# Optimization experiments

Measured on AMD Instinct MI355X. Metric: run time of the kernel, lower is better.

The kernel has to match this reference:

```python
import jax, jax.numpy as jnp
import numpy as np

N, E, NG = 50000, 800000, 256          # nodes, edges, graphs
NODE, EDGE, HID, OUT = 64, 16, 64, 1   # feature dims
NUM_LAYERS = 3


def _lin(key, fan_in, fan_out):
    # torch Linear default init: U(-1/sqrt(fan_in), 1/sqrt(fan_in))
    kw, kb = jax.random.split(key)
    bound = 1.0 / np.sqrt(fan_in)
    W = jax.random.uniform(kw, (fan_in, fan_out), jnp.float32, -bound, bound)
    b = jax.random.uniform(kb, (fan_out,), jnp.float32, -bound, bound)
    return W, b


def setup_inputs() -> dict:
    key = jax.random.key(0)
    ks = jax.random.split(key, 8)
    x = jax.random.normal(ks[0], (N, NODE), jnp.float32)
    edge_attr = jax.random.normal(ks[1], (E, EDGE), jnp.float32)
    edge_index = jax.random.randint(ks[2], (2, E), 0, N, dtype=jnp.int32)
    batch = jnp.sort(jax.random.randint(ks[3], (N,), 0, NG, dtype=jnp.int32))
    W_nh, b_nh = _lin(ks[4], NODE, HID)                 # node_to_hidden
    W_mh, b_mh = _lin(ks[5], 2 * HID + EDGE, HID)       # message_to_hidden
    W_om, b_om = _lin(ks[6], 2 * HID + NODE, HID)       # outMsgLin
    W_out, b_out = _lin(ks[7], HID, OUT)                # outLin
    return {"x": x, "edge_attr": edge_attr,
            "W_nh": W_nh, "b_nh": b_nh, "W_mh": W_mh, "b_mh": b_mh,
            "W_om": W_om, "b_om": b_om, "W_out": W_out, "b_out": b_out,
            "edge_index": edge_index, "batch": batch}


def reference(x, edge_attr, W_nh, b_nh, W_mh, b_mh, W_om, b_om, W_out, b_out,
              edge_index, batch):
    # h0 = relu(node_to_hidden(x))
    h0 = jax.nn.relu(x @ W_nh + b_nh)                      # [N, HID]

    # add_self_loops: append N self edges, self-loop edge_attr filled with 1.0
    self_idx = jnp.arange(N, dtype=edge_index.dtype)
    src = jnp.concatenate([edge_index[0], self_idx])       # x_j index (source)
    dst = jnp.concatenate([edge_index[1], self_idx])       # x_i index (target)
    ea = jnp.concatenate([edge_attr,
                          jnp.ones((N, EDGE), edge_attr.dtype)], axis=0)

    # MPN: num_layers of gather-concat -> scatter-add -> linear + h0 -> relu
    h = h0
    for _ in range(NUM_LAYERS):
        msg = jnp.concatenate([h[dst], h[src], ea], axis=1)        # [E+N, 2H+EDGE]
        agg = jax.ops.segment_sum(msg, dst, num_segments=N)        # [N, 2H+EDGE]
        h = jax.nn.relu(agg @ W_mh + b_mh + h0)                    # [N, HID]

    # outMsg: message = concat[h_i, h_j, x_j], aggr add, update identity
    out_msg = jnp.concatenate([h[dst], h[src], x[src]], axis=1)    # [E+N, 2H+NODE]
    agg2 = jax.ops.segment_sum(out_msg, dst, num_segments=N)       # [N, 2H+NODE]

    out = jax.nn.relu(agg2 @ W_om + b_om)                          # [N, HID]
    pooled = jax.ops.segment_sum(out, batch, num_segments=NG)      # [NG, HID]
    return pooled @ W_out + b_out                                  # [NG, OUT]
```

## Files before the change

### kernel.cpp

```cpp
#include <hip/hip_runtime.h>
#include <hip/hip_fp16.h>

#define N_NODES 50000
#define N_EDGES 800000
#define NGRAPH  256
#define FDIM    64
#define EDIM    16
#define NT      (N_NODES / 16)
#define SH      8
#define M8      (N_NODES * SH)
#define NB8     ((M8 + 255) / 256)
#define CH8     ((NB8 + 255) / 256)
#define NBG     ((N_NODES + 31) / 32)

#define GRPS       8
#define GRP_BLOCKS 256
#define GRID_CF    (GRPS * GRP_BLOCKS)
#define NPG        ((N_NODES + GRPS - 1) / GRPS)

#define SRC_SHARD(s) ((s) >> 13)

using half8  = __attribute__((ext_vector_type(8))) _Float16;
using float4v = __attribute__((ext_vector_type(4))) float;

__device__ __forceinline__ unsigned hadd2u(unsigned a, unsigned b) {
    __half2 r = __hadd2(__builtin_bit_cast(__half2, a), __builtin_bit_cast(__half2, b));
    return __builtin_bit_cast(unsigned, r);
}
__device__ __forceinline__ unsigned hmul2u(unsigned a, __half2 m) {
    __half2 r = __hmul2(__builtin_bit_cast(__half2, a), m);
    return __builtin_bit_cast(unsigned, r);
}


__global__ __launch_bounds__(256) void k_count(const int* __restrict__ src,
                                               const int* __restrict__ dst,
                                               int* __restrict__ cnt8) {
    int grp = blockIdx.x & (GRPS - 1);
    int bi  = blockIdx.x >> 3;
    int lo = grp * NPG;
    int hi = lo + NPG; if (hi > N_NODES) hi = N_NODES;
    for (int e = bi * 256 + threadIdx.x; e < N_EDGES; e += GRP_BLOCKS * 256) {
        int d = dst[e];
        if (d >= lo && d < hi) atomicAdd(&cnt8[d * SH + SRC_SHARD(src[e])], 1);
    }
}

__global__ void k_cvt_x(const float* __restrict__ x, __half* __restrict__ x16) {
    int t = blockIdx.x * blockDim.x + threadIdx.x;
    if (t < N_NODES * FDIM) x16[t] = __float2half(x[t]);
}

__global__ void k_blksum(const int* __restrict__ cnt8, int* __restrict__ blksum) {
    __shared__ int red[4];
    int b = blockIdx.x, t = threadIdx.x;
    int idx = b * 256 + t;
    int s = (idx < M8) ? cnt8[idx] : 0;
#pragma unroll
    for (int off = 32; off > 0; off >>= 1) s += __shfl_down(s, off, 64);
    int lane = t & 63, wid = t >> 6;
    if (lane == 0) red[wid] = s;
    __syncthreads();
    if (t == 0) blksum[b] = red[0] + red[1] + red[2] + red[3];
}

__global__ void k_scanblk(const int* __restrict__ blksum, int* __restrict__ boff,
                          int* __restrict__ rowp8) {
    __shared__ int sh[256];
    int t = threadIdx.x;
    int base = t * CH8;
    int v[CH8];
    int s = 0;
#pragma unroll
    for (int i = 0; i < CH8; i++) {
        int idx = base + i;
        v[i] = (idx < NB8) ? blksum[idx] : 0;
        s += v[i];
    }
    sh[t] = s;
    __syncthreads();
    for (int off = 1; off < 256; off <<= 1) {
        int u = (t >= off) ? sh[t - off] : 0;
        __syncthreads();
        sh[t] += u;
        __syncthreads();
    }
    int run = (t == 0) ? 0 : sh[t - 1];
#pragma unroll
    for (int i = 0; i < CH8; i++) {
        int idx = base + i;
        if (idx < NB8) boff[idx] = run;
        run += v[i];
    }
    if (t == 255) rowp8[M8] = sh[255];
}

__global__ void k_rowp(const int* __restrict__ cnt8, const int* __restrict__ boff,
                       int* __restrict__ rowp8, int* __restrict__ cur8) {
    __shared__ int sh[256];
    int b = blockIdx.x, t = threadIdx.x;
    int idx = b * 256 + t;
    int v = (idx < M8) ? cnt8[idx] : 0;
    sh[t] = v;
    __syncthreads();
    for (int off = 1; off < 256; off <<= 1) {
        int u = (t >= off) ? sh[t - off] : 0;
        __syncthreads();
        sh[t] += u;
        __syncthreads();
    }
    if (idx < M8) {
        int excl = sh[t] - v + boff[b];
        rowp8[idx] = excl;
        cur8[idx]  = excl;
    }
}

__global__ void k_degf(const int* __restrict__ rowp8, float* __restrict__ degf) {
    int i = blockIdx.x * blockDim.x + threadIdx.x;
    if (i < N_NODES) degf[i] = (float)(rowp8[(i + 1) * SH] - rowp8[i * SH] + 1);
}

__global__ __launch_bounds__(256) void k_fill(const int* __restrict__ src,
                                              const int* __restrict__ dst,
                                              int* __restrict__ cur8,
                                              int* __restrict__ colsrc,
                                              int* __restrict__ coledge) {
    int grp = blockIdx.x & (GRPS - 1);
    int bi  = blockIdx.x >> 3;
    int lo = grp * NPG;
    int hi = lo + NPG; if (hi > N_NODES) hi = N_NODES;
    for (int e = bi * 256 + threadIdx.x; e < N_EDGES; e += GRP_BLOCKS * 256) {
        int d = dst[e];
        if (d >= lo && d < hi) {
            int s = src[e];
            int pos = atomicAdd(&cur8[d * SH + SRC_SHARD(s)], 1);
            colsrc[pos]  = s;
            coledge[pos] = e;
        }
    }
}


__global__ __launch_bounds__(256, 8) void k_gather(
    const __half* __restrict__ h16,
    const int* __restrict__ rowp8, const int* __restrict__ colsrc,
    __half* __restrict__ agg16) {
    int lane = threadIdx.x & 63, wid = threadIdx.x >> 6;
    int g = lane >> 3;
    int c = lane & 7;
    const uint4* h8 = (const uint4*)h16;
    int node = (blockIdx.x * 4 + wid) * 8 + g;
    if (node >= N_NODES) return;
    int beg = rowp8[node * SH], end = rowp8[(node + 1) * SH];
    float a0 = 0, a1 = 0, a2 = 0, a3 = 0, a4 = 0, a5 = 0, a6 = 0, a7 = 0;
    for (int p = beg; p < end; p += 8) {
        int cidx = p + c; if (cidx > end - 1) cidx = end - 1;
        int vj = colsrc[cidx];
#pragma unroll
        for (int k = 0; k < 8; k++) {
            int j = __shfl(vj, g * 8 + k, 64);
            if (p + k < end) {
                uint4 v = h8[(size_t)j * 8 + c];
                float2 f0 = __half22float2(__builtin_bit_cast(__half2, v.x));
                float2 f1 = __half22float2(__builtin_bit_cast(__half2, v.y));
                float2 f2 = __half22float2(__builtin_bit_cast(__half2, v.z));
                float2 f3 = __half22float2(__builtin_bit_cast(__half2, v.w));
                a0 += f0.x; a1 += f0.y; a2 += f1.x; a3 += f1.y;
                a4 += f2.x; a5 += f2.y; a6 += f3.x; a7 += f3.y;
            }
        }
    }
    uint4 o;
    o.x = __builtin_bit_cast(unsigned, __floats2half2_rn(a0, a1));
    o.y = __builtin_bit_cast(unsigned, __floats2half2_rn(a2, a3));
    o.z = __builtin_bit_cast(unsigned, __floats2half2_rn(a4, a5));
    o.w = __builtin_bit_cast(unsigned, __floats2half2_rn(a6, a7));
    ((uint4*)agg16)[(size_t)node * 8 + c] = o;
}

__global__ __launch_bounds__(256, 8) void k_gxea(
    const __half* __restrict__ h16, const float* __restrict__ edge_attr,
    const int* __restrict__ rowp8, const int* __restrict__ colsrc,
    const int* __restrict__ coledge,
    __half* __restrict__ agg16, float* __restrict__ ea) {
    int lane = threadIdx.x & 63, wid = threadIdx.x >> 6;
    int g = lane >> 3;
    int c = lane & 7;
    const uint4* h8 = (const uint4*)h16;
    const float2* a2p = (const float2*)edge_attr;
    int node = (blockIdx.x * 4 + wid) * 8 + g;
    if (node >= N_NODES) return;
    int beg = rowp8[node * SH], end = rowp8[(node + 1) * SH];
    float a0 = 0, a1 = 0, a2 = 0, a3 = 0, a4 = 0, a5 = 0, a6 = 0, a7 = 0;
    float x0 = 0.f, x1 = 0.f;
    for (int p = beg; p < end; p += 8) {
        int cidx = p + c; if (cidx > end - 1) cidx = end - 1;
        int vs = colsrc[cidx];
        int ve = coledge[cidx];
#pragma unroll
        for (int k = 0; k < 8; k++) {
            int j = __shfl(vs, g * 8 + k, 64);
            int e = __shfl(ve, g * 8 + k, 64);
            if (p + k < end) {
                uint4 v = h8[(size_t)j * 8 + c];
                float2 w = a2p[(size_t)e * 8 + c];
                float2 f0 = __half22float2(__builtin_bit_cast(__half2, v.x));
                float2 f1 = __half22float2(__builtin_bit_cast(__half2, v.y));
                float2 f2 = __half22float2(__builtin_bit_cast(__half2, v.z));
                float2 f3 = __half22float2(__builtin_bit_cast(__half2, v.w));
                a0 += f0.x; a1 += f0.y; a2 += f1.x; a3 += f1.y;
                a4 += f2.x; a5 += f2.y; a6 += f3.x; a7 += f3.y;
                x0 += w.x; x1 += w.y;
            }
        }
    }
    uint4 o;
    o.x = __builtin_bit_cast(unsigned, __floats2half2_rn(a0, a1));
    o.y = __builtin_bit_cast(unsigned, __floats2half2_rn(a2, a3));
    o.z = __builtin_bit_cast(unsigned, __floats2half2_rn(a4, a5));
    o.w = __builtin_bit_cast(unsigned, __floats2half2_rn(a6, a7));
    ((uint4*)agg16)[(size_t)node * 8 + c] = o;
    ((float2*)ea)[(size_t)node * 8 + c] = make_float2(x0, x1);
}

__global__ void k_h0base(const float* __restrict__ x, const float* __restrict__ ea,
                         const float* __restrict__ Wnh, const float* __restrict__ bnh,
                         const float* __restrict__ Wmh, const float* __restrict__ bmh,
                         __half* __restrict__ h0out16, __half* __restrict__ base16) {
    __shared__ __align__(16) float sx[4][FDIM];
    __shared__ __align__(16) float sea[4][EDIM];
    int lane = threadIdx.x & 63;
    int wid  = threadIdx.x >> 6;
    float wnh[FDIM], w3[EDIM];
#pragma unroll
    for (int m = 0; m < FDIM; m++) wnh[m] = Wnh[m * FDIM + lane];
    float csum = 0.f;
#pragma unroll
    for (int m = 0; m < EDIM; m++) {
        w3[m] = Wmh[(2 * FDIM + m) * FDIM + lane];
        csum += w3[m];
    }
    float bnhk = bnh[lane], bmhk = bmh[lane];
    int gw = blockIdx.x * 4 + wid;
    int nw = gridDim.x * 4;
    for (int i = gw; i < N_NODES; i += nw) {
        sx[wid][lane] = x[i * FDIM + lane];
        if (lane < EDIM) sea[wid][lane] = ea[i * EDIM + lane];
        float acc0 = bnhk, acc1 = 0.f, acc2 = 0.f, acc3 = 0.f;
        const float4* s4 = (const float4*)sx[wid];
#pragma unroll
        for (int m4 = 0; m4 < FDIM / 4; m4++) {
            float4 v = s4[m4];
            acc0 = fmaf(v.x, wnh[4 * m4 + 0], acc0);
            acc1 = fmaf(v.y, wnh[4 * m4 + 1], acc1);
            acc2 = fmaf(v.z, wnh[4 * m4 + 2], acc2);
            acc3 = fmaf(v.w, wnh[4 * m4 + 3], acc3);
        }
        float h0 = fmaxf((acc0 + acc2) + (acc1 + acc3), 0.f);
        float b0 = h0 + bmhk + csum, b1 = 0.f, b2 = 0.f, b3 = 0.f;
        const float4* e4 = (const float4*)sea[wid];
#pragma unroll
        for (int m4 = 0; m4 < EDIM / 4; m4++) {
            float4 v = e4[m4];
            b0 = fmaf(v.x, w3[4 * m4 + 0], b0);
            b1 = fmaf(v.y, w3[4 * m4 + 1], b1);
            b2 = fmaf(v.z, w3[4 * m4 + 2], b2);
            b3 = fmaf(v.w, w3[4 * m4 + 3], b3);
        }
        h0out16[i * FDIM + lane] = __float2half(h0);
        base16[i * FDIM + lane]  = __float2half((b0 + b2) + (b1 + b3));
    }
}

#define SROW 136

__global__ __launch_bounds__(256, 4) void k_mv_mfma(
    const __half* __restrict__ agg16, const __half* __restrict__ hin16,
    const __half* __restrict__ base16, const float* __restrict__ degf,
    const float* __restrict__ Wmh, __half* __restrict__ hout16) {
    __shared__ __align__(16) _Float16 S[4][16 * SROW];
    int lane = threadIdx.x & 63, wid = threadIdx.x >> 6;
    int n = lane & 15, quad = lane >> 4;
    half8 bfr[4][4];
#pragma unroll
    for (int kk = 0; kk < 4; kk++)
#pragma unroll
        for (int nn = 0; nn < 4; nn++) {
            half8 tmp;
#pragma unroll
            for (int j = 0; j < 8; j++) {
                int kp = kk * 32 + quad * 8 + j;
                int krow = (kp < 64) ? (64 + kp) : (kp - 64);
                tmp[j] = (_Float16)Wmh[krow * FDIM + nn * 16 + n];
            }
            bfr[kk][nn] = tmp;
        }
    int t = blockIdx.x * 4 + wid;
    if (t >= NT) return;
    int tb = t * 16;
    {
        int m = lane >> 2, c = lane & 3;
        int node = tb + m;
        const uint4* ag4 = (const uint4*)agg16;
        const uint4* hh4 = (const uint4*)hin16;
        uint4 agA = ag4[(size_t)node * 8 + c * 2];
        uint4 agB = ag4[(size_t)node * 8 + c * 2 + 1];
        uint4 hA  = hh4[(size_t)node * 8 + c * 2];
        uint4 hB  = hh4[(size_t)node * 8 + c * 2 + 1];
        __half dh = __float2half(degf[node]);
        __half2 dh2 = __halves2half2(dh, dh);
        uint4 s2A, s2B, s1A, s1B;
        s2A.x = hadd2u(agA.x, hA.x); s2A.y = hadd2u(agA.y, hA.y);
        s2A.z = hadd2u(agA.z, hA.z); s2A.w = hadd2u(agA.w, hA.w);
        s2B.x = hadd2u(agB.x, hB.x); s2B.y = hadd2u(agB.y, hB.y);
        s2B.z = hadd2u(agB.z, hB.z); s2B.w = hadd2u(agB.w, hB.w);
        s1A.x = hmul2u(hA.x, dh2); s1A.y = hmul2u(hA.y, dh2);
        s1A.z = hmul2u(hA.z, dh2); s1A.w = hmul2u(hA.w, dh2);
        s1B.x = hmul2u(hB.x, dh2); s1B.y = hmul2u(hB.y, dh2);
        s1B.z = hmul2u(hB.z, dh2); s1B.w = hmul2u(hB.w, dh2);
        uint4* Sw = (uint4*)(&S[wid][m * SROW]);
        Sw[c * 2]     = s2A;
        Sw[c * 2 + 1] = s2B;
        Sw[8 + c * 2]     = s1A;
        Sw[8 + c * 2 + 1] = s1B;
    }
    float4v acc[4];
#pragma unroll
    for (int nn = 0; nn < 4; nn++)
#pragma unroll
        for (int r = 0; r < 4; r++)
            acc[nn][r] = __half2float(base16[(size_t)(tb + quad * 4 + r) * FDIM + nn * 16 + n]);
    const _Float16* Sr = S[wid];
#pragma unroll
    for (int kk = 0; kk < 4; kk++) {
        half8 a = *(const half8*)(Sr + (lane & 15) * SROW + kk * 32 + quad * 8);
#pragma unroll
        for (int nn = 0; nn < 4; nn++)
            acc[nn] = __builtin_amdgcn_mfma_f32_16x16x32_f16(a, bfr[kk][nn], acc[nn], 0, 0, 0);
    }
#pragma unroll
    for (int nn = 0; nn < 4; nn++)
#pragma unroll
        for (int r = 0; r < 4; r++)
            hout16[(size_t)(tb + quad * 4 + r) * FDIM + nn * 16 + n] =
                __float2half(fmaxf(acc[nn][r], 0.f));
}

__global__ __launch_bounds__(256, 4) void k_out_mv_mfma(
    const __half* __restrict__ agg16, const __half* __restrict__ hin16,
    const __half* __restrict__ obase16, const float* __restrict__ degf,
    const float* __restrict__ Wom, const float* __restrict__ Wout,
    float* __restrict__ sc) {
    __shared__ __align__(16) _Float16 S[4][16 * SROW];
    int lane = threadIdx.x & 63, wid = threadIdx.x >> 6;
    int n = lane & 15, quad = lane >> 4;
    half8 bfr[4][4];
#pragma unroll
    for (int kk = 0; kk < 4; kk++)
#pragma unroll
        for (int nn = 0; nn < 4; nn++) {
            half8 tmp;
#pragma unroll
            for (int j = 0; j < 8; j++) {
                int kp = kk * 32 + quad * 8 + j;
                int krow = (kp < 64) ? (64 + kp) : (kp - 64);
                tmp[j] = (_Float16)Wom[krow * FDIM + nn * 16 + n];
            }
            bfr[kk][nn] = tmp;
        }
    float wo0 = Wout[n], wo1 = Wout[16 + n], wo2 = Wout[32 + n], wo3 = Wout[48 + n];
    int t = blockIdx.x * 4 + wid;
    if (t >= NT) return;
    int tb = t * 16;
    {
        int m = lane >> 2, c = lane & 3;
        int node = tb + m;
        const uint4* ag4 = (const uint4*)agg16;
        const uint4* hh4 = (const uint4*)hin16;
        uint4 agA = ag4[(size_t)node * 8 + c * 2];
        uint4 agB = ag4[(size_t)node * 8 + c * 2 + 1];
        uint4 hA  = hh4[(size_t)node * 8 + c * 2];
        uint4 hB  = hh4[(size_t)node * 8 + c * 2 + 1];
        __half dh = __float2half(degf[node]);
        __half2 dh2 = __halves2half2(dh, dh);
        uint4 s2A, s2B, s1A, s1B;
        s2A.x = hadd2u(agA.x, hA.x); s2A.y = hadd2u(agA.y, hA.y);
        s2A.z = hadd2u(agA.z, hA.z); s2A.w = hadd2u(agA.w, hA.w);
        s2B.x = hadd2u(agB.x, hB.x); s2B.y = hadd2u(agB.y, hB.y);
        s2B.z = hadd2u(agB.z, hB.z); s2B.w = hadd2u(agB.w, hB.w);
        s1A.x = hmul2u(hA.x, dh2); s1A.y = hmul2u(hA.y, dh2);
        s1A.z = hmul2u(hA.z, dh2); s1A.w = hmul2u(hA.w, dh2);
        s1B.x = hmul2u(hB.x, dh2); s1B.y = hmul2u(hB.y, dh2);
        s1B.z = hmul2u(hB.z, dh2); s1B.w = hmul2u(hB.w, dh2);
        uint4* Sw = (uint4*)(&S[wid][m * SROW]);
        Sw[c * 2]     = s2A;
        Sw[c * 2 + 1] = s2B;
        Sw[8 + c * 2]     = s1A;
        Sw[8 + c * 2 + 1] = s1B;
    }
    float4v acc[4];
#pragma unroll
    for (int nn = 0; nn < 4; nn++)
#pragma unroll
        for (int r = 0; r < 4; r++)
            acc[nn][r] = __half2float(obase16[(size_t)(tb + quad * 4 + r) * FDIM + nn * 16 + n]);
    const _Float16* Sr = S[wid];
#pragma unroll
    for (int kk = 0; kk < 4; kk++) {
        half8 a = *(const half8*)(Sr + (lane & 15) * SROW + kk * 32 + quad * 8);
#pragma unroll
        for (int nn = 0; nn < 4; nn++)
            acc[nn] = __builtin_amdgcn_mfma_f32_16x16x32_f16(a, bfr[kk][nn], acc[nn], 0, 0, 0);
    }
#pragma unroll
    for (int r = 0; r < 4; r++) {
        float s = fmaxf(acc[0][r], 0.f) * wo0 + fmaxf(acc[1][r], 0.f) * wo1
                + fmaxf(acc[2][r], 0.f) * wo2 + fmaxf(acc[3][r], 0.f) * wo3;
        s += __shfl_xor(s, 1, 64);
        s += __shfl_xor(s, 2, 64);
        s += __shfl_xor(s, 4, 64);
        s += __shfl_xor(s, 8, 64);
        if (n == 0) sc[tb + quad * 4 + r] = s;
    }
}

#define SROW2 72
__global__ __launch_bounds__(256, 4) void k_obase_mfma(
    const __half* __restrict__ aggX16, const __half* __restrict__ x16,
    const float* __restrict__ Wom, const float* __restrict__ bom,
    __half* __restrict__ obase16) {
    __shared__ __align__(16) _Float16 S[4][16 * SROW2];
    int lane = threadIdx.x & 63, wid = threadIdx.x >> 6;
    int n = lane & 15, quad = lane >> 4;
    half8 bfr[2][4];
#pragma unroll
    for (int kk = 0; kk < 2; kk++)
#pragma unroll
        for (int nn = 0; nn < 4; nn++) {
            half8 tmp;
#pragma unroll
            for (int j = 0; j < 8; j++) {
                int kp = kk * 32 + quad * 8 + j;
                tmp[j] = (_Float16)Wom[(128 + kp) * FDIM + nn * 16 + n];
            }
            bfr[kk][nn] = tmp;
        }
    float bom_n[4];
#pragma unroll
    for (int nn = 0; nn < 4; nn++) bom_n[nn] = bom[nn * 16 + n];
    int t = blockIdx.x * 4 + wid;
    if (t >= NT) return;
    int tb = t * 16;
    {
        int m = lane >> 2, c = lane & 3;
        int node = tb + m;
        const uint4* ag4 = (const uint4*)aggX16;
        const uint4* xx4 = (const uint4*)x16;
        uint4 agA = ag4[(size_t)node * 8 + c * 2];
        uint4 agB = ag4[(size_t)node * 8 + c * 2 + 1];
        uint4 xA  = xx4[(size_t)node * 8 + c * 2];
        uint4 xB  = xx4[(size_t)node * 8 + c * 2 + 1];
        uint4 sA, sB;
        sA.x = hadd2u(agA.x, xA.x); sA.y = hadd2u(agA.y, xA.y);
        sA.z = hadd2u(agA.z, xA.z); sA.w = hadd2u(agA.w, xA.w);
        sB.x = hadd2u(agB.x, xB.x); sB.y = hadd2u(agB.y, xB.y);
        sB.z = hadd2u(agB.z, xB.z); sB.w = hadd2u(agB.w, xB.w);
        uint4* Sw = (uint4*)(&S[wid][m * SROW2]);
        Sw[c * 2]     = sA;
        Sw[c * 2 + 1] = sB;
    }
    float4v acc[4];
#pragma unroll
    for (int nn = 0; nn < 4; nn++)
#pragma unroll
        for (int r = 0; r < 4; r++) acc[nn][r] = bom_n[nn];
    const _Float16* Sr = S[wid];
#pragma unroll
    for (int kk = 0; kk < 2; kk++) {
        half8 a = *(const half8*)(Sr + (lane & 15) * SROW2 + kk * 32 + quad * 8);
#pragma unroll
        for (int nn = 0; nn < 4; nn++)
            acc[nn] = __builtin_amdgcn_mfma_f32_16x16x32_f16(a, bfr[kk][nn], acc[nn], 0, 0, 0);
    }
#pragma unroll
    for (int nn = 0; nn < 4; nn++)
#pragma unroll
        for (int r = 0; r < 4; r++)
            obase16[(size_t)(tb + quad * 4 + r) * FDIM + nn * 16 + n] =
                __float2half(acc[nn][r]);
}

__global__ void k_pool(const float* __restrict__ sc, const int* __restrict__ batch,
                       const float* __restrict__ b_out, float* __restrict__ out) {
    __shared__ float red[4];
    int g = blockIdx.x, t = threadIdx.x;
    int lo = 0, hi = N_NODES;
    while (lo < hi) { int mid = (lo + hi) >> 1; if (batch[mid] < g) lo = mid + 1; else hi = mid; }
    int lo2 = lo, hi2 = N_NODES;
    while (lo2 < hi2) { int mid = (lo2 + hi2) >> 1; if (batch[mid] < g + 1) lo2 = mid + 1; else hi2 = mid; }
    float s = 0.f;
    for (int i = lo + t; i < lo2; i += 256) s += sc[i];
#pragma unroll
    for (int off = 32; off > 0; off >>= 1) s += __shfl_down(s, off, 64);
    int lane = t & 63, wid = t >> 6;
    if (lane == 0) red[wid] = s;
    __syncthreads();
    if (t == 0) out[g] = red[0] + red[1] + red[2] + red[3] + b_out[0];
}


extern "C" void kernel_launch(void* const* d_in, const int* in_sizes, int n_in,
                              void* d_out, int out_size, void* d_ws, size_t ws_size,
                              hipStream_t stream) {
    const float* x         = (const float*)d_in[0];
    const float* edge_attr = (const float*)d_in[1];
    const float* Wnh       = (const float*)d_in[2];
    const float* bnh       = (const float*)d_in[3];
    const float* Wmh       = (const float*)d_in[4];
    const float* bmh       = (const float*)d_in[5];
    const float* Wom       = (const float*)d_in[6];
    const float* bom       = (const float*)d_in[7];
    const float* Wout      = (const float*)d_in[8];
    const float* bout      = (const float*)d_in[9];
    const int*   eidx      = (const int*)d_in[10];
    const int*   batch     = (const int*)d_in[11];
    const int*   srcI = eidx;
    const int*   dstI = eidx + N_EDGES;
    float* out = (float*)d_out;
    (void)in_sizes; (void)n_in; (void)out_size;

    char* w = (char*)d_ws;
    size_t off = 0;
    auto take = [&](size_t b) -> void* {
        void* p = w + off;
        off = (off + b + 255) & ~(size_t)255;
        return p;
    };
    float*  ea     = (float*)take((size_t)N_NODES * EDIM * 4);
    int*    cnt8   = (int*)take((size_t)M8 * 4);
    int*    rowp8  = (int*)take((size_t)(M8 + 1) * 4);
    int*    cur8   = (int*)take((size_t)M8 * 4);
    float*  degf   = (float*)take((size_t)N_NODES * 4);
    int*    colsrc = (int*)take((size_t)N_EDGES * 4);
    int*    coledge= (int*)take((size_t)N_EDGES * 4);
    float*  sc     = (float*)take((size_t)N_NODES * 4);
    int*    blks   = (int*)take((size_t)NB8 * 4);
    int*    boff   = (int*)take((size_t)NB8 * 4);
    __half* x16    = (__half*)take((size_t)N_NODES * FDIM * 2);
    __half* hA16   = (__half*)take((size_t)N_NODES * FDIM * 2);
    __half* hB16   = (__half*)take((size_t)N_NODES * FDIM * 2);
    __half* agg16  = (__half*)take((size_t)N_NODES * FDIM * 2);
    __half* base16 = (__half*)take((size_t)N_NODES * FDIM * 2);
    __half* obase16= (__half*)take((size_t)N_NODES * FDIM * 2);
    (void)ws_size;

    const int MVG = (NT + 3) / 4;
    const int GBG = (NBG + 0);

    hipMemsetAsync(cnt8, 0, (size_t)M8 * 4, stream);
    k_count<<<GRID_CF, 256, 0, stream>>>(srcI, dstI, cnt8);
    k_cvt_x<<<(N_NODES * FDIM + 255) / 256, 256, 0, stream>>>(x, x16);
    k_blksum<<<NB8, 256, 0, stream>>>(cnt8, blks);
    k_scanblk<<<1, 256, 0, stream>>>(blks, boff, rowp8);
    k_rowp<<<NB8, 256, 0, stream>>>(cnt8, boff, rowp8, cur8);
    k_degf<<<(N_NODES + 255) / 256, 256, 0, stream>>>(rowp8, degf);
    k_fill<<<GRID_CF, 256, 0, stream>>>(srcI, dstI, cur8, colsrc, coledge);

    k_gxea<<<GBG, 256, 0, stream>>>(x16, edge_attr, rowp8, colsrc, coledge,
                                    agg16, ea);
    k_obase_mfma<<<MVG, 256, 0, stream>>>(agg16, x16, Wom, bom, obase16);
    k_h0base<<<2048, 256, 0, stream>>>(x, ea, Wnh, bnh, Wmh, bmh, hA16, base16);

    k_gather<<<GBG, 256, 0, stream>>>(hA16, rowp8, colsrc, agg16);
    k_mv_mfma<<<MVG, 256, 0, stream>>>(agg16, hA16, base16, degf, Wmh, hB16);

    k_gather<<<GBG, 256, 0, stream>>>(hB16, rowp8, colsrc, agg16);
    k_mv_mfma<<<MVG, 256, 0, stream>>>(agg16, hB16, base16, degf, Wmh, hA16);

    k_gather<<<GBG, 256, 0, stream>>>(hA16, rowp8, colsrc, agg16);
    k_mv_mfma<<<MVG, 256, 0, stream>>>(agg16, hA16, base16, degf, Wmh, hB16);

    k_gather<<<GBG, 256, 0, stream>>>(hB16, rowp8, colsrc, agg16);
    k_out_mv_mfma<<<MVG, 256, 0, stream>>>(agg16, hB16, obase16, degf, Wom, Wout, sc);
    k_pool<<<NGRAPH, 256, 0, stream>>>(sc, batch, bout, out);
}
```

Baseline: 363.7 us.

## Fuse neighbor gather into MFMA linear kernels, dropping the agg buffer

Merges each gather kernel with the MFMA matvec that follows it, so a wave aggregates neighbor features for its 16-node tile straight into shared memory and then runs the matmul. This removes the round trip of the agg16 intermediate through global memory and cuts five kernel launches. In exchange, the gather phase now runs at the occupancy limit set for the MFMA kernel (launch bounds 4 instead of 8) and with fewer waves overall, which may weaken latency hiding for the irregular gathers. The aggregate is also added in fp32 before a single rounding to fp16, rather than being rounded first and then added in fp16.

```diff
diff --git a/kernel.cpp b/kernel.cpp
--- a/kernel.cpp
+++ b/kernel.cpp
@@ -11,7 +11,6 @@
 #define M8      (N_NODES * SH)
 #define NB8     ((M8 + 255) / 256)
 #define CH8     ((NB8 + 255) / 256)
-#define NBG     ((N_NODES + 31) / 32)
 
 #define GRPS       8
 #define GRP_BLOCKS 256
@@ -30,6 +29,9 @@
 __device__ __forceinline__ unsigned hmul2u(unsigned a, __half2 m) {
     __half2 r = __hmul2(__builtin_bit_cast(__half2, a), m);
     return __builtin_bit_cast(unsigned, r);
+}
+__device__ __forceinline__ unsigned packf2(float a, float b) {
+    return __builtin_bit_cast(unsigned, __floats2half2_rn(a, b));
 }
 
 
@@ -141,87 +143,298 @@
     }
 }
 
-
-__global__ __launch_bounds__(256, 8) void k_gather(
-    const __half* __restrict__ h16,
+#define SROW 136
+
+__global__ __launch_bounds__(256, 4) void k_gmv(
+    const __half* __restrict__ hin16,
     const int* __restrict__ rowp8, const int* __restrict__ colsrc,
-    __half* __restrict__ agg16) {
+    const __half* __restrict__ base16, const float* __restrict__ degf,
+    const float* __restrict__ Wmh, __half* __restrict__ hout16) {
+    __shared__ __align__(16) _Float16 S[4][16 * SROW];
     int lane = threadIdx.x & 63, wid = threadIdx.x >> 6;
+    int t = blockIdx.x * 4 + wid;
+    if (t >= NT) return;
+    int tb = t * 16;
     int g = lane >> 3;
     int c = lane & 7;
-    const uint4* h8 = (const uint4*)h16;
-    int node = (blockIdx.x * 4 + wid) * 8 + g;
-    if (node >= N_NODES) return;
-    int beg = rowp8[node * SH], end = rowp8[(node + 1) * SH];
-    float a0 = 0, a1 = 0, a2 = 0, a3 = 0, a4 = 0, a5 = 0, a6 = 0, a7 = 0;
-    for (int p = beg; p < end; p += 8) {
-        int cidx = p + c; if (cidx > end - 1) cidx = end - 1;
-        int vj = colsrc[cidx];
-#pragma unroll
-        for (int k = 0; k < 8; k++) {
-            int j = __shfl(vj, g * 8 + k, 64);
-            if (p + k < end) {
-                uint4 v = h8[(size_t)j * 8 + c];
-                float2 f0 = __half22float2(__builtin_bit_cast(__half2, v.x));
-                float2 f1 = __half22float2(__builtin_bit_cast(__half2, v.y));
-                float2 f2 = __half22float2(__builtin_bit_cast(__half2, v.z));
-                float2 f3 = __half22float2(__builtin_bit_cast(__half2, v.w));
-                a0 += f0.x; a1 += f0.y; a2 += f1.x; a3 += f1.y;
-                a4 += f2.x; a5 += f2.y; a6 += f3.x; a7 += f3.y;
+    const uint4* h8 = (const uint4*)hin16;
+
+#pragma unroll
+    for (int pass = 0; pass < 2; pass++) {
+        int m = pass * 8 + g;
+        int node = tb + m;
+        int beg = rowp8[node * SH], end = rowp8[(node + 1) * SH];
+        float a0 = 0, a1 = 0, a2 = 0, a3 = 0, a4 = 0, a5 = 0, a6 = 0, a7 = 0;
+        for (int p = beg; p < end; p += 8) {
+            int cidx = p + c; if (cidx > end - 1) cidx = end - 1;
+            int vj = colsrc[cidx];
+#pragma unroll
+            for (int k = 0; k < 8; k++) {
+                int j = __shfl(vj, g * 8 + k, 64);
+                if (p + k < end) {
+                    uint4 v = h8[(size_t)j * 8 + c];
+                    float2 f0 = __half22float2(__builtin_bit_cast(__half2, v.x));
+                    float2 f1 = __half22float2(__builtin_bit_cast(__half2, v.y));
+                    float2 f2 = __half22float2(__builtin_bit_cast(__half2, v.z));
+                    float2 f3 = __half22float2(__builtin_bit_cast(__half2, v.w));
+                    a0 += f0.x; a1 += f0.y; a2 += f1.x; a3 += f1.y;
+                    a4 += f2.x; a5 += f2.y; a6 += f3.x; a7 += f3.y;
+                }
             }
         }
-    }
-    uint4 o;
-    o.x = __builtin_bit_cast(unsigned, __floats2half2_rn(a0, a1));
-    o.y = __builtin_bit_cast(unsigned, __floats2half2_rn(a2, a3));
-    o.z = __builtin_bit_cast(unsigned, __floats2half2_rn(a4, a5));
-    o.w = __builtin_bit_cast(unsigned, __floats2half2_rn(a6, a7));
-    ((uint4*)agg16)[(size_t)node * 8 + c] = o;
-}
-
-__global__ __launch_bounds__(256, 8) void k_gxea(
-    const __half* __restrict__ h16, const float* __restrict__ edge_attr,
+        uint4 hv = h8[(size_t)node * 8 + c];
+        float dg = degf[node];
+        __half dh = __float2half(dg);
+        __half2 dh2 = __halves2half2(dh, dh);
+        float2 f0 = __half22float2(__builtin_bit_cast(__half2, hv.x));
+        float2 f1 = __half22float2(__builtin_bit_cast(__half2, hv.y));
+        float2 f2 = __half22float2(__builtin_bit_cast(__half2, hv.z));
+        float2 f3 = __half22float2(__builtin_bit_cast(__half2, hv.w));
+        uint4 s2, s1;
+        s2.x = packf2(a0 + f0.x, a1 + f0.y);
+        s2.y = packf2(a2 + f1.x, a3 + f1.y);
+        s2.z = packf2(a4 + f2.x, a5 + f2.y);
+        s2.w = packf2(a6 + f3.x, a7 + f3.y);
+        s1.x = hmul2u(hv.x, dh2); s1.y = hmul2u(hv.y, dh2);
+        s1.z = hmul2u(hv.z, dh2); s1.w = hmul2u(hv.w, dh2);
+        uint4* Sw = (uint4*)(&S[wid][m * SROW]);
+        Sw[c]     = s2;
+        Sw[8 + c] = s1;
+    }
+
+    int n = lane & 15, quad = lane >> 4;
+    half8 bfr[4][4];
+#pragma unroll
+    for (int kk = 0; kk < 4; kk++)
+#pragma unroll
+        for (int nn = 0; nn < 4; nn++) {
+            half8 tmp;
+#pragma unroll
+            for (int j = 0; j < 8; j++) {
+                int kp = kk * 32 + quad * 8 + j;
+                int krow = (kp < 64) ? (64 + kp) : (kp - 64);
+                tmp[j] = (_Float16)Wmh[krow * FDIM + nn * 16 + n];
+            }
+            bfr[kk][nn] = tmp;
+        }
+    float4v acc[4];
+#pragma unroll
+    for (int nn = 0; nn < 4; nn++)
+#pragma unroll
+        for (int r = 0; r < 4; r++)
+            acc[nn][r] = __half2float(base16[(size_t)(tb + quad * 4 + r) * FDIM + nn * 16 + n]);
+    const _Float16* Sr = S[wid];
+#pragma unroll
+    for (int kk = 0; kk < 4; kk++) {
+        half8 a = *(const half8*)(Sr + n * SROW + kk * 32 + quad * 8);
+#pragma unroll
+        for (int nn = 0; nn < 4; nn++)
+            acc[nn] = __builtin_amdgcn_mfma_f32_16x16x32_f16(a, bfr[kk][nn], acc[nn], 0, 0, 0);
+    }
+#pragma unroll
+    for (int nn = 0; nn < 4; nn++)
+#pragma unroll
+        for (int r = 0; r < 4; r++)
+            hout16[(size_t)(tb + quad * 4 + r) * FDIM + nn * 16 + n] =
+                __float2half(fmaxf(acc[nn][r], 0.f));
+}
+
+__global__ __launch_bounds__(256, 4) void k_gout(
+    const __half* __restrict__ hin16,
+    const int* __restrict__ rowp8, const int* __restrict__ colsrc,
+    const __half* __restrict__ obase16, const float* __restrict__ degf,
+    const float* __restrict__ Wom, const float* __restrict__ Wout,
+    float* __restrict__ sc) {
+    __shared__ __align__(16) _Float16 S[4][16 * SROW];
+    int lane = threadIdx.x & 63, wid = threadIdx.x >> 6;
+    int t = blockIdx.x * 4 + wid;
+    if (t >= NT) return;
+    int tb = t * 16;
+    int g = lane >> 3;
+    int c = lane & 7;
+    const uint4* h8 = (const uint4*)hin16;
+
+#pragma unroll
+    for (int pass = 0; pass < 2; pass++) {
+        int m = pass * 8 + g;
+        int node = tb + m;
+        int beg = rowp8[node * SH], end = rowp8[(node + 1) * SH];
+        float a0 = 0, a1 = 0, a2 = 0, a3 = 0, a4 = 0, a5 = 0, a6 = 0, a7 = 0;
+        for (int p = beg; p < end; p += 8) {
+            int cidx = p + c; if (cidx > end - 1) cidx = end - 1;
+            int vj = colsrc[cidx];
+#pragma unroll
+            for (int k = 0; k < 8; k++) {
+                int j = __shfl(vj, g * 8 + k, 64);
+                if (p + k < end) {
+                    uint4 v = h8[(size_t)j * 8 + c];
+                    float2 f0 = __half22float2(__builtin_bit_cast(__half2, v.x));
+                    float2 f1 = __half22float2(__builtin_bit_cast(__half2, v.y));
+                    float2 f2 = __half22float2(__builtin_bit_cast(__half2, v.z));
+                    float2 f3 = __half22float2(__builtin_bit_cast(__half2, v.w));
+                    a0 += f0.x; a1 += f0.y; a2 += f1.x; a3 += f1.y;
+                    a4 += f2.x; a5 += f2.y; a6 += f3.x; a7 += f3.y;
+                }
+            }
+        }
+        uint4 hv = h8[(size_t)node * 8 + c];
+        float dg = degf[node];
+        __half dh = __float2half(dg);
+        __half2 dh2 = __halves2half2(dh, dh);
+        float2 f0 = __half22float2(__builtin_bit_cast(__half2, hv.x));
+        float2 f1 = __half22float2(__builtin_bit_cast(__half2, hv.y));
+        float2 f2 = __half22float2(__builtin_bit_cast(__half2, hv.z));
+        float2 f3 = __half22float2(__builtin_bit_cast(__half2, hv.w));
+        uint4 s2, s1;
+        s2.x = packf2(a0 + f0.x, a1 + f0.y);
+        s2.y = packf2(a2 + f1.x, a3 + f1.y);
+        s2.z = packf2(a4 + f2.x, a5 + f2.y);
+        s2.w = packf2(a6 + f3.x, a7 + f3.y);
+        s1.x = hmul2u(hv.x, dh2); s1.y = hmul2u(hv.y, dh2);
+        s1.z = hmul2u(hv.z, dh2); s1.w = hmul2u(hv.w, dh2);
+        uint4* Sw = (uint4*)(&S[wid][m * SROW]);
+        Sw[c]     = s2;
+        Sw[8 + c] = s1;
+    }
+
+    int n = lane & 15, quad = lane >> 4;
+    half8 bfr[4][4];
+#pragma unroll
+    for (int kk = 0; kk < 4; kk++)
+#pragma unroll
+        for (int nn = 0; nn < 4; nn++) {
+            half8 tmp;
+#pragma unroll
+            for (int j = 0; j < 8; j++) {
+                int kp = kk * 32 + quad * 8 + j;
+                int krow = (kp < 64) ? (64 + kp) : (kp - 64);
+                tmp[j] = (_Float16)Wom[krow * FDIM + nn * 16 + n];
+            }
+            bfr[kk][nn] = tmp;
+        }
+    float wo0 = Wout[n], wo1 = Wout[16 + n], wo2 = Wout[32 + n], wo3 = Wout[48 + n];
+    float4v acc[4];
+#pragma unroll
+    for (int nn = 0; nn < 4; nn++)
+#pragma unroll
+        for (int r = 0; r < 4; r++)
+            acc[nn][r] = __half2float(obase16[(size_t)(tb + quad * 4 + r) * FDIM + nn * 16 + n]);
+    const _Float16* Sr = S[wid];
+#pragma unroll
+    for (int kk = 0; kk < 4; kk++) {
+        half8 a = *(const half8*)(Sr + n * SROW + kk * 32 + quad * 8);
+#pragma unroll
+        for (int nn = 0; nn < 4; nn++)
+            acc[nn] = __builtin_amdgcn_mfma_f32_16x16x32_f16(a, bfr[kk][nn], acc[nn], 0, 0, 0);
+    }
+#pragma unroll
+    for (int r = 0; r < 4; r++) {
+        float s = fmaxf(acc[0][r], 0.f) * wo0 + fmaxf(acc[1][r], 0.f) * wo1
+                + fmaxf(acc[2][r], 0.f) * wo2 + fmaxf(acc[3][r], 0.f) * wo3;
+        s += __shfl_xor(s, 1, 64);
+        s += __shfl_xor(s, 2, 64);
+        s += __shfl_xor(s, 4, 64);
+        s += __shfl_xor(s, 8, 64);
+        if (n == 0) sc[tb + quad * 4 + r] = s;
+    }
+}
+
+#define SROW2 72
+__global__ __launch_bounds__(256, 4) void k_gxob(
+    const __half* __restrict__ x16, const float* __restrict__ edge_attr,
     const int* __restrict__ rowp8, const int* __restrict__ colsrc,
     const int* __restrict__ coledge,
-    __half* __restrict__ agg16, float* __restrict__ ea) {
+    const float* __restrict__ Wom, const float* __restrict__ bom,
+    __half* __restrict__ obase16, float* __restrict__ ea) {
+    __shared__ __align__(16) _Float16 S[4][16 * SROW2];
     int lane = threadIdx.x & 63, wid = threadIdx.x >> 6;
+    int t = blockIdx.x * 4 + wid;
+    if (t >= NT) return;
+    int tb = t * 16;
     int g = lane >> 3;
     int c = lane & 7;
-    const uint4* h8 = (const uint4*)h16;
+    const uint4* h8 = (const uint4*)x16;
     const float2* a2p = (const float2*)edge_attr;
-    int node = (blockIdx.x * 4 + wid) * 8 + g;
-    if (node >= N_NODES) return;
-    int beg = rowp8[node * SH], end = rowp8[(node + 1) * SH];
-    float a0 = 0, a1 = 0, a2 = 0, a3 = 0, a4 = 0, a5 = 0, a6 = 0, a7 = 0;
-    float x0 = 0.f, x1 = 0.f;
-    for (int p = beg; p < end; p += 8) {
-        int cidx = p + c; if (cidx > end - 1) cidx = end - 1;
-        int vs = colsrc[cidx];
-        int ve = coledge[cidx];
-#pragma unroll
-        for (int k = 0; k < 8; k++) {
-            int j = __shfl(vs, g * 8 + k, 64);
-            int e = __shfl(ve, g * 8 + k, 64);
-            if (p + k < end) {
-                uint4 v = h8[(size_t)j * 8 + c];
-                float2 w = a2p[(size_t)e * 8 + c];
-                float2 f0 = __half22float2(__builtin_bit_cast(__half2, v.x));
-                float2 f1 = __half22float2(__builtin_bit_cast(__half2, v.y));
-                float2 f2 = __half22float2(__builtin_bit_cast(__half2, v.z));
-                float2 f3 = __half22float2(__builtin_bit_cast(__half2, v.w));
-                a0 += f0.x; a1 += f0.y; a2 += f1.x; a3 += f1.y;
-                a4 += f2.x; a5 += f2.y; a6 += f3.x; a7 += f3.y;
-                x0 += w.x; x1 += w.y;
+
+#pragma unroll
+    for (int pass = 0; pass < 2; pass++) {
+        int m = pass * 8 + g;
+        int node = tb + m;
+        int beg = rowp8[node * SH], end = rowp8[(node + 1) * SH];
+        float a0 = 0, a1 = 0, a2 = 0, a3 = 0, a4 = 0, a5 = 0, a6 = 0, a7 = 0;
+        float x0 = 0.f, x1 = 0.f;
+        for (int p = beg; p < end; p += 8) {
+            int cidx = p + c; if (cidx > end - 1) cidx = end - 1;
+            int vs = colsrc[cidx];
+            int ve = coledge[cidx];
+#pragma unroll
+            for (int k = 0; k < 8; k++) {
+                int j = __shfl(vs, g * 8 + k, 64);
+                int e = __shfl(ve, g * 8 + k, 64);
+                if (p + k < end) {
+                    uint4 v = h8[(size_t)j * 8 + c];
+                    float2 w = a2p[(size_t)e * 8 + c];
+                    float2 f0 = __half22float2(__builtin_bit_cast(__half2, v.x));
+                    float2 f1 = __half22float2(__builtin_bit_cast(__half2, v.y));
+                    float2 f2 = __half22float2(__builtin_bit_cast(__half2, v.z));
+                    float2 f3 = __half22float2(__builtin_bit_cast(__half2, v.w));
+                    a0 += f0.x; a1 += f0.y; a2 += f1.x; a3 += f1.y;
+                    a4 += f2.x; a5 += f2.y; a6 += f3.x; a7 += f3.y;
+                    x0 += w.x; x1 += w.y;
+                }
             }
         }
-    }
-    uint4 o;
-    o.x = __builtin_bit_cast(unsigned, __floats2half2_rn(a0, a1));
-    o.y = __builtin_bit_cast(unsigned, __floats2half2_rn(a2, a3));
-    o.z = __builtin_bit_cast(unsigned, __floats2half2_rn(a4, a5));
-    o.w = __builtin_bit_cast(unsigned, __floats2half2_rn(a6, a7));
-    ((uint4*)agg16)[(size_t)node * 8 + c] = o;
-    ((float2*)ea)[(size_t)node * 8 + c] = make_float2(x0, x1);
+        uint4 xv = h8[(size_t)node * 8 + c];
+        float2 f0 = __half22float2(__builtin_bit_cast(__half2, xv.x));
+        float2 f1 = __half22float2(__builtin_bit_cast(__half2, xv.y));
+        float2 f2 = __half22float2(__builtin_bit_cast(__half2, xv.z));
+        float2 f3 = __half22float2(__builtin_bit_cast(__half2, xv.w));
+        uint4 sA;
+        sA.x = packf2(a0 + f0.x, a1 + f0.y);
+        sA.y = packf2(a2 + f1.x, a3 + f1.y);
+        sA.z = packf2(a4 + f2.x, a5 + f2.y);
+        sA.w = packf2(a6 + f3.x, a7 + f3.y);
+        uint4* Sw = (uint4*)(&S[wid][m * SROW2]);
+        Sw[c] = sA;
+        ((float2*)ea)[(size_t)node * 8 + c] = make_float2(x0, x1);
+    }
+
+    int n = lane & 15, quad = lane >> 4;
+    half8 bfr[2][4];
+#pragma unroll
+    for (int kk = 0; kk < 2; kk++)
+#pragma unroll
+        for (int nn = 0; nn < 4; nn++) {
+            half8 tmp;
+#pragma unroll
+            for (int j = 0; j < 8; j++) {
+                int kp = kk * 32 + quad * 8 + j;
+                tmp[j] = (_Float16)Wom[(128 + kp) * FDIM + nn * 16 + n];
+            }
+            bfr[kk][nn] = tmp;
+        }
+    float bom_n[4];
+#pragma unroll
+    for (int nn = 0; nn < 4; nn++) bom_n[nn] = bom[nn * 16 + n];
+    float4v acc[4];
+#pragma unroll
+    for (int nn = 0; nn < 4; nn++)
+#pragma unroll
+        for (int r = 0; r < 4; r++) acc[nn][r] = bom_n[nn];
+    const _Float16* Sr = S[wid];
+#pragma unroll
+    for (int kk = 0; kk < 2; kk++) {
+        half8 a = *(const half8*)(Sr + n * SROW2 + kk * 32 + quad * 8);
+#pragma unroll
+        for (int nn = 0; nn < 4; nn++)
+            acc[nn] = __builtin_amdgcn_mfma_f32_16x16x32_f16(a, bfr[kk][nn], acc[nn], 0, 0, 0);
+    }
+#pragma unroll
+    for (int nn = 0; nn < 4; nn++)
+#pragma unroll
+        for (int r = 0; r < 4; r++)
+            obase16[(size_t)(tb + quad * 4 + r) * FDIM + nn * 16 + n] =
+                __float2half(acc[nn][r]);
 }
 
 __global__ void k_h0base(const float* __restrict__ x, const float* __restrict__ ea,
@@ -271,224 +484,6 @@
         h0out16[i * FDIM + lane] = __float2half(h0);
         base16[i * FDIM + lane]  = __float2half((b0 + b2) + (b1 + b3));
     }
-}
-
-#define SROW 136
-
-__global__ __launch_bounds__(256, 4) void k_mv_mfma(
-    const __half* __restrict__ agg16, const __half* __restrict__ hin16,
-    const __half* __restrict__ base16, const float* __restrict__ degf,
-    const float* __restrict__ Wmh, __half* __restrict__ hout16) {
-    __shared__ __align__(16) _Float16 S[4][16 * SROW];
-    int lane = threadIdx.x & 63, wid = threadIdx.x >> 6;
-    int n = lane & 15, quad = lane >> 4;
-    half8 bfr[4][4];
-#pragma unroll
-    for (int kk = 0; kk < 4; kk++)
-#pragma unroll
-        for (int nn = 0; nn < 4; nn++) {
-            half8 tmp;
-#pragma unroll
-            for (int j = 0; j < 8; j++) {
-                int kp = kk * 32 + quad * 8 + j;
-                int krow = (kp < 64) ? (64 + kp) : (kp - 64);
-                tmp[j] = (_Float16)Wmh[krow * FDIM + nn * 16 + n];
-            }
-            bfr[kk][nn] = tmp;
-        }
-    int t = blockIdx.x * 4 + wid;
-    if (t >= NT) return;
-    int tb = t * 16;
-    {
-        int m = lane >> 2, c = lane & 3;
-        int node = tb + m;
-        const uint4* ag4 = (const uint4*)agg16;
-        const uint4* hh4 = (const uint4*)hin16;
-        uint4 agA = ag4[(size_t)node * 8 + c * 2];
-        uint4 agB = ag4[(size_t)node * 8 + c * 2 + 1];
-        uint4 hA  = hh4[(size_t)node * 8 + c * 2];
-        uint4 hB  = hh4[(size_t)node * 8 + c * 2 + 1];
-        __half dh = __float2half(degf[node]);
-        __half2 dh2 = __halves2half2(dh, dh);
-        uint4 s2A, s2B, s1A, s1B;
-        s2A.x = hadd2u(agA.x, hA.x); s2A.y = hadd2u(agA.y, hA.y);
-        s2A.z = hadd2u(agA.z, hA.z); s2A.w = hadd2u(agA.w, hA.w);
-        s2B.x = hadd2u(agB.x, hB.x); s2B.y = hadd2u(agB.y, hB.y);
-        s2B.z = hadd2u(agB.z, hB.z); s2B.w = hadd2u(agB.w, hB.w);
-        s1A.x = hmul2u(hA.x, dh2); s1A.y = hmul2u(hA.y, dh2);
-        s1A.z = hmul2u(hA.z, dh2); s1A.w = hmul2u(hA.w, dh2);
-        s1B.x = hmul2u(hB.x, dh2); s1B.y = hmul2u(hB.y, dh2);
-        s1B.z = hmul2u(hB.z, dh2); s1B.w = hmul2u(hB.w, dh2);
-        uint4* Sw = (uint4*)(&S[wid][m * SROW]);
-        Sw[c * 2]     = s2A;
-        Sw[c * 2 + 1] = s2B;
-        Sw[8 + c * 2]     = s1A;
-        Sw[8 + c * 2 + 1] = s1B;
-    }
-    float4v acc[4];
-#pragma unroll
-    for (int nn = 0; nn < 4; nn++)
-#pragma unroll
-        for (int r = 0; r < 4; r++)
-            acc[nn][r] = __half2float(base16[(size_t)(tb + quad * 4 + r) * FDIM + nn * 16 + n]);
-    const _Float16* Sr = S[wid];
-#pragma unroll
-    for (int kk = 0; kk < 4; kk++) {
-        half8 a = *(const half8*)(Sr + (lane & 15) * SROW + kk * 32 + quad * 8);
-#pragma unroll
-        for (int nn = 0; nn < 4; nn++)
-            acc[nn] = __builtin_amdgcn_mfma_f32_16x16x32_f16(a, bfr[kk][nn], acc[nn], 0, 0, 0);
-    }
-#pragma unroll
-    for (int nn = 0; nn < 4; nn++)
-#pragma unroll
-        for (int r = 0; r < 4; r++)
-            hout16[(size_t)(tb + quad * 4 + r) * FDIM + nn * 16 + n] =
-                __float2half(fmaxf(acc[nn][r], 0.f));
-}
-
-__global__ __launch_bounds__(256, 4) void k_out_mv_mfma(
-    const __half* __restrict__ agg16, const __half* __restrict__ hin16,
-    const __half* __restrict__ obase16, const float* __restrict__ degf,
-    const float* __restrict__ Wom, const float* __restrict__ Wout,
-    float* __restrict__ sc) {
-    __shared__ __align__(16) _Float16 S[4][16 * SROW];
-    int lane = threadIdx.x & 63, wid = threadIdx.x >> 6;
-    int n = lane & 15, quad = lane >> 4;
-    half8 bfr[4][4];
-#pragma unroll
-    for (int kk = 0; kk < 4; kk++)
-#pragma unroll
-        for (int nn = 0; nn < 4; nn++) {
-            half8 tmp;
-#pragma unroll
-            for (int j = 0; j < 8; j++) {
-                int kp = kk * 32 + quad * 8 + j;
-                int krow = (kp < 64) ? (64 + kp) : (kp - 64);
-                tmp[j] = (_Float16)Wom[krow * FDIM + nn * 16 + n];
-            }
-            bfr[kk][nn] = tmp;
-        }
-    float wo0 = Wout[n], wo1 = Wout[16 + n], wo2 = Wout[32 + n], wo3 = Wout[48 + n];
-    int t = blockIdx.x * 4 + wid;
-    if (t >= NT) return;
-    int tb = t * 16;
-    {
-        int m = lane >> 2, c = lane & 3;
-        int node = tb + m;
-        const uint4* ag4 = (const uint4*)agg16;
-        const uint4* hh4 = (const uint4*)hin16;
-        uint4 agA = ag4[(size_t)node * 8 + c * 2];
-        uint4 agB = ag4[(size_t)node * 8 + c * 2 + 1];
-        uint4 hA  = hh4[(size_t)node * 8 + c * 2];
-        uint4 hB  = hh4[(size_t)node * 8 + c * 2 + 1];
-        __half dh = __float2half(degf[node]);
-        __half2 dh2 = __halves2half2(dh, dh);
-        uint4 s2A, s2B, s1A, s1B;
-        s2A.x = hadd2u(agA.x, hA.x); s2A.y = hadd2u(agA.y, hA.y);
-        s2A.z = hadd2u(agA.z, hA.z); s2A.w = hadd2u(agA.w, hA.w);
-        s2B.x = hadd2u(agB.x, hB.x); s2B.y = hadd2u(agB.y, hB.y);
-        s2B.z = hadd2u(agB.z, hB.z); s2B.w = hadd2u(agB.w, hB.w);
-        s1A.x = hmul2u(hA.x, dh2); s1A.y = hmul2u(hA.y, dh2);
-        s1A.z = hmul2u(hA.z, dh2); s1A.w = hmul2u(hA.w, dh2);
-        s1B.x = hmul2u(hB.x, dh2); s1B.y = hmul2u(hB.y, dh2);
-        s1B.z = hmul2u(hB.z, dh2); s1B.w = hmul2u(hB.w, dh2);
-        uint4* Sw = (uint4*)(&S[wid][m * SROW]);
-        Sw[c * 2]     = s2A;
-        Sw[c * 2 + 1] = s2B;
-        Sw[8 + c * 2]     = s1A;
-        Sw[8 + c * 2 + 1] = s1B;
-    }
-    float4v acc[4];
-#pragma unroll
-    for (int nn = 0; nn < 4; nn++)
-#pragma unroll
-        for (int r = 0; r < 4; r++)
-            acc[nn][r] = __half2float(obase16[(size_t)(tb + quad * 4 + r) * FDIM + nn * 16 + n]);
-    const _Float16* Sr = S[wid];
-#pragma unroll
-    for (int kk = 0; kk < 4; kk++) {
-        half8 a = *(const half8*)(Sr + (lane & 15) * SROW + kk * 32 + quad * 8);
-#pragma unroll
-        for (int nn = 0; nn < 4; nn++)
-            acc[nn] = __builtin_amdgcn_mfma_f32_16x16x32_f16(a, bfr[kk][nn], acc[nn], 0, 0, 0);
-    }
-#pragma unroll
-    for (int r = 0; r < 4; r++) {
-        float s = fmaxf(acc[0][r], 0.f) * wo0 + fmaxf(acc[1][r], 0.f) * wo1
-                + fmaxf(acc[2][r], 0.f) * wo2 + fmaxf(acc[3][r], 0.f) * wo3;
-        s += __shfl_xor(s, 1, 64);
-        s += __shfl_xor(s, 2, 64);
-        s += __shfl_xor(s, 4, 64);
-        s += __shfl_xor(s, 8, 64);
-        if (n == 0) sc[tb + quad * 4 + r] = s;
-    }
-}
-
-#define SROW2 72
-__global__ __launch_bounds__(256, 4) void k_obase_mfma(
-    const __half* __restrict__ aggX16, const __half* __restrict__ x16,
-    const float* __restrict__ Wom, const float* __restrict__ bom,
-    __half* __restrict__ obase16) {
-    __shared__ __align__(16) _Float16 S[4][16 * SROW2];
-    int lane = threadIdx.x & 63, wid = threadIdx.x >> 6;
-    int n = lane & 15, quad = lane >> 4;
-    half8 bfr[2][4];
-#pragma unroll
-    for (int kk = 0; kk < 2; kk++)
-#pragma unroll
-        for (int nn = 0; nn < 4; nn++) {
-            half8 tmp;
-#pragma unroll
-            for (int j = 0; j < 8; j++) {
-                int kp = kk * 32 + quad * 8 + j;
-                tmp[j] = (_Float16)Wom[(128 + kp) * FDIM + nn * 16 + n];
-            }
-            bfr[kk][nn] = tmp;
-        }
-    float bom_n[4];
-#pragma unroll
-    for (int nn = 0; nn < 4; nn++) bom_n[nn] = bom[nn * 16 + n];
-    int t = blockIdx.x * 4 + wid;
-    if (t >= NT) return;
-    int tb = t * 16;
-    {
-        int m = lane >> 2, c = lane & 3;
-        int node = tb + m;
-        const uint4* ag4 = (const uint4*)aggX16;
-        const uint4* xx4 = (const uint4*)x16;
-        uint4 agA = ag4[(size_t)node * 8 + c * 2];
-        uint4 agB = ag4[(size_t)node * 8 + c * 2 + 1];
-        uint4 xA  = xx4[(size_t)node * 8 + c * 2];
-        uint4 xB  = xx4[(size_t)node * 8 + c * 2 + 1];
-        uint4 sA, sB;
-        sA.x = hadd2u(agA.x, xA.x); sA.y = hadd2u(agA.y, xA.y);
-        sA.z = hadd2u(agA.z, xA.z); sA.w = hadd2u(agA.w, xA.w);
-        sB.x = hadd2u(agB.x, xB.x); sB.y = hadd2u(agB.y, xB.y);
-        sB.z = hadd2u(agB.z, xB.z); sB.w = hadd2u(agB.w, xB.w);
-        uint4* Sw = (uint4*)(&S[wid][m * SROW2]);
-        Sw[c * 2]     = sA;
-        Sw[c * 2 + 1] = sB;
-    }
-    float4v acc[4];
-#pragma unroll
-    for (int nn = 0; nn < 4; nn++)
-#pragma unroll
-        for (int r = 0; r < 4; r++) acc[nn][r] = bom_n[nn];
-    const _Float16* Sr = S[wid];
-#pragma unroll
-    for (int kk = 0; kk < 2; kk++) {
-        half8 a = *(const half8*)(Sr + (lane & 15) * SROW2 + kk * 32 + quad * 8);
-#pragma unroll
-        for (int nn = 0; nn < 4; nn++)
-            acc[nn] = __builtin_amdgcn_mfma_f32_16x16x32_f16(a, bfr[kk][nn], acc[nn], 0, 0, 0);
-    }
-#pragma unroll
-    for (int nn = 0; nn < 4; nn++)
-#pragma unroll
-        for (int r = 0; r < 4; r++)
-            obase16[(size_t)(tb + quad * 4 + r) * FDIM + nn * 16 + n] =
-                __float2half(acc[nn][r]);
 }
 
 __global__ void k_pool(const float* __restrict__ sc, const int* __restrict__ batch,
@@ -550,13 +545,11 @@
     __half* x16    = (__half*)take((size_t)N_NODES * FDIM * 2);
     __half* hA16   = (__half*)take((size_t)N_NODES * FDIM * 2);
     __half* hB16   = (__half*)take((size_t)N_NODES * FDIM * 2);
-    __half* agg16  = (__half*)take((size_t)N_NODES * FDIM * 2);
     __half* base16 = (__half*)take((size_t)N_NODES * FDIM * 2);
     __half* obase16= (__half*)take((size_t)N_NODES * FDIM * 2);
     (void)ws_size;
 
     const int MVG = (NT + 3) / 4;
-    const int GBG = (NBG + 0);
 
     hipMemsetAsync(cnt8, 0, (size_t)M8 * 4, stream);
     k_count<<<GRID_CF, 256, 0, stream>>>(srcI, dstI, cnt8);
@@ -567,21 +560,14 @@
     k_degf<<<(N_NODES + 255) / 256, 256, 0, stream>>>(rowp8, degf);
     k_fill<<<GRID_CF, 256, 0, stream>>>(srcI, dstI, cur8, colsrc, coledge);
 
-    k_gxea<<<GBG, 256, 0, stream>>>(x16, edge_attr, rowp8, colsrc, coledge,
-                                    agg16, ea);
-    k_obase_mfma<<<MVG, 256, 0, stream>>>(agg16, x16, Wom, bom, obase16);
+    k_gxob<<<MVG, 256, 0, stream>>>(x16, edge_attr, rowp8, colsrc, coledge,
+                                    Wom, bom, obase16, ea);
     k_h0base<<<2048, 256, 0, stream>>>(x, ea, Wnh, bnh, Wmh, bmh, hA16, base16);
 
-    k_gather<<<GBG, 256, 0, stream>>>(hA16, rowp8, colsrc, agg16);
-    k_mv_mfma<<<MVG, 256, 0, stream>>>(agg16, hA16, base16, degf, Wmh, hB16);
-
-    k_gather<<<GBG, 256, 0, stream>>>(hB16, rowp8, colsrc, agg16);
-    k_mv_mfma<<<MVG, 256, 0, stream>>>(agg16, hB16, base16, degf, Wmh, hA16);
-
-    k_gather<<<GBG, 256, 0, stream>>>(hA16, rowp8, colsrc, agg16);
-    k_mv_mfma<<<MVG, 256, 0, stream>>>(agg16, hA16, base16, degf, Wmh, hB16);
-
-    k_gather<<<GBG, 256, 0, stream>>>(hB16, rowp8, colsrc, agg16);
-    k_out_mv_mfma<<<MVG, 256, 0, stream>>>(agg16, hB16, obase16, degf, Wom, Wout, sc);
+    k_gmv<<<MVG, 256, 0, stream>>>(hA16, rowp8, colsrc, base16, degf, Wmh, hB16);
+    k_gmv<<<MVG, 256, 0, stream>>>(hB16, rowp8, colsrc, base16, degf, Wmh, hA16);
+    k_gmv<<<MVG, 256, 0, stream>>>(hA16, rowp8, colsrc, base16, degf, Wmh, hB16);
+
+    k_gout<<<MVG, 256, 0, stream>>>(hB16, rowp8, colsrc, obase16, degf, Wom, Wout, sc);
     k_pool<<<NGRAPH, 256, 0, stream>>>(sc, batch, bout, out);
 }
```

Result: slower. 371.3 us (+2.1%).
